# Performance work log

Measured on AMD Instinct MI355X. Metric: run time of the kernel, lower is better.

The kernel has to match this reference:

```python
import jax, jax.numpy as jnp
import numpy as np

HEADS = 8
DIM_HEAD = 64  # note: per-head dim is inner_dim/heads = 512 due to the module's inner_dim = dim_head*dim
SCALE = DIM_HEAD ** (-0.5)
EPS = 1e-5


def layernorm(x, gamma):
    # nn.LayerNorm(dim, elementwise_affine=False) then x * (gamma + 1)
    mu = jnp.mean(x, axis=-1, keepdims=True)
    var = jnp.var(x, axis=-1, keepdims=True)
    xn = (x - mu) * jax.lax.rsqrt(var + EPS)
    return xn * (gamma + 1.0)


def setup_inputs() -> dict:
    key = jax.random.key(0)
    ks = jax.random.split(key, 6)
    b, n, dim = 2, 2048, 256
    inner = DIM_HEAD * dim  # 4096
    x = jax.random.normal(ks[0], (b, n, dim), dtype=jnp.float32)
    gamma = jax.random.normal(ks[1], (dim,), dtype=jnp.float32) * 0.02
    Wq = jax.random.normal(ks[2], (inner, dim), dtype=jnp.float32) * 0.02
    Wk = jax.random.normal(ks[3], (inner, dim), dtype=jnp.float32) * 0.02
    Wv = jax.random.normal(ks[4], (inner, dim), dtype=jnp.float32) * 0.02
    Wo = jax.random.normal(ks[5], (dim, inner), dtype=jnp.float32) * 0.02
    return {"x": x, "gamma": gamma, "Wq": Wq, "Wk": Wk, "Wv": Wv, "Wo": Wo}


def reference(x, gamma, Wq, Wk, Wv, Wo):
    b, n, dim = x.shape
    h = HEADS
    xn = layernorm(x, gamma)  # reuse_attention=True -> norm = LayerNorm(dim)
    # self-attention: context = xn (cross_attend=False, norm_context=Identity)
    q = jnp.einsum('bnd,ed->bne', xn, Wq).reshape(b, n, h, -1).transpose(0, 2, 1, 3)
    k = jnp.einsum('bnd,ed->bne', xn, Wk).reshape(b, n, h, -1).transpose(0, 2, 1, 3)
    v = jnp.einsum('bnd,ed->bne', xn, Wv).reshape(b, n, h, -1).transpose(0, 2, 1, 3)
    qk_sim = jnp.einsum('bhqd,bhkd->bhqk', q * SCALE, k)
    attn = jax.nn.softmax(qk_sim, axis=-1)  # dropout p=0.0 -> identity
    dot = jnp.einsum('bhqk,bhkd->bhqd', attn, v)
    out = dot.transpose(0, 2, 1, 3).reshape(b, n, -1)
    out = jnp.einsum('bne,de->bnd', out, Wo)
    return out
```

## Files before the change

### kernel.cpp

```cpp
#include <hip/hip_runtime.h>


typedef unsigned short u16;
typedef unsigned int u32;
typedef __bf16 bf16x8 __attribute__((ext_vector_type(8)));
typedef float f32x4 __attribute__((ext_vector_type(4)));

__device__ __forceinline__ u16 f2bf(float f) {
    u32 u = __builtin_bit_cast(u32, f);
    u += 0x7fffu + ((u >> 16) & 1u);
    return (u16)(u >> 16);
}

#define GLDS16(G, L)                                                                  \
    __builtin_amdgcn_global_load_lds((const __attribute__((address_space(1))) u32*)(G), \
                                     (__attribute__((address_space(3))) u32*)(L), 16, 0, 0)

template <typename OutT, bool ATOMIC>
__global__ void __launch_bounds__(256, 4) gemm_bt(
    const u16* __restrict__ A, const u16* __restrict__ B, OutT* __restrict__ C,
    int K, int lda, int ldb, int ldc,
    long sAh, long sAb, long sBh, long sBb, long sCh, long sCb,
    int H, int NB, long ksA, long ksB)
{
    __shared__ u16 ldsA[128 * 32];
    __shared__ u16 ldsB[128 * 32];

    const int z = blockIdx.z;
    const int zh = z % H;
    const int zq = z / H;
    const int zb = zq % NB;
    const int kc = zq / NB;
    A += (size_t)zh * sAh + (size_t)zb * sAb + (size_t)kc * ksA;
    B += (size_t)zh * sBh + (size_t)zb * sBb + (size_t)kc * ksB;
    C += (size_t)zh * sCh + (size_t)zb * sCb;

    const int bm = blockIdx.y * 128;
    const int bn = blockIdx.x * 128;
    const int t = threadIdx.x;
    const int w = t >> 6, l = t & 63;
    const int wm = w >> 1, wn = w & 1;
    const int lr = l & 15, lk = l >> 4;
    const int sw = lk ^ ((lr >> 1) & 3);

    const int m0 = t >> 2, s0 = t & 3;
    const int c0 = s0 ^ ((m0 >> 1) & 3);
    const int m1 = 64 + m0;
    const int c1 = s0 ^ ((m1 >> 1) & 3);

    const u16* gA0 = A + (size_t)(bm + m0) * lda + c0 * 8;
    const u16* gA1 = A + (size_t)(bm + m1) * lda + c1 * 8;
    const u16* gB0 = B + (size_t)(bn + m0) * ldb + c0 * 8;
    const u16* gB1 = B + (size_t)(bn + m1) * ldb + c1 * 8;
    u16* lA0 = &ldsA[(t & ~63) * 8];
    u16* lA1 = &ldsA[(256 + (t & ~63)) * 8];
    u16* lB0 = &ldsB[(t & ~63) * 8];
    u16* lB1 = &ldsB[(256 + (t & ~63)) * 8];

    f32x4 acc[4][4];
#pragma unroll
    for (int i = 0; i < 4; ++i)
#pragma unroll
        for (int j = 0; j < 4; ++j)
            acc[i][j] = f32x4{0.f, 0.f, 0.f, 0.f};

    const int nk = K >> 5;
    for (int kt = 0; kt < nk; ++kt) {
        __syncthreads();
        GLDS16(gA0, lA0); GLDS16(gA1, lA1);
        GLDS16(gB0, lB0); GLDS16(gB1, lB1);
        gA0 += 32; gA1 += 32; gB0 += 32; gB1 += 32;
        __syncthreads();

        bf16x8 av[4], bv[4];
#pragma unroll
        for (int i = 0; i < 4; ++i) {
            av[i] = *(const bf16x8*)&ldsA[(wm * 64 + i * 16 + lr) * 32 + sw * 8];
            bv[i] = *(const bf16x8*)&ldsB[(wn * 64 + i * 16 + lr) * 32 + sw * 8];
        }
#pragma unroll
        for (int i = 0; i < 4; ++i)
#pragma unroll
            for (int j = 0; j < 4; ++j)
                acc[i][j] = __builtin_amdgcn_mfma_f32_16x16x32_bf16(av[i], bv[j], acc[i][j], 0, 0, 0);
    }

#pragma unroll
    for (int i = 0; i < 4; ++i) {
        const int row0 = bm + wm * 64 + i * 16 + lk * 4;
#pragma unroll
        for (int j = 0; j < 4; ++j) {
            const int col = bn + wn * 64 + j * 16 + lr;
#pragma unroll
            for (int r = 0; r < 4; ++r) {
                const size_t idx = (size_t)(row0 + r) * ldc + col;
                const float v = acc[i][j][r];
                if constexpr (ATOMIC) {
                    atomicAdd(&C[idx], v);
                } else if constexpr (sizeof(OutT) == 2) {
                    C[idx] = (OutT)f2bf(v);
                } else {
                    C[idx] = (OutT)v;
                }
            }
        }
    }
}

__global__ void __launch_bounds__(256, 2) attn_fused(
    const u16* __restrict__ Y, const u16* __restrict__ xn,
    const u16* __restrict__ Zt, float* __restrict__ out)
{
    __shared__ u16 ldsY[8 * 64 * 32];
    __shared__ u16 ldsB[128 * 32];
    __shared__ u16 ldsZ[256 * 32];
    __shared__ u16 Pl[64 * 136];
    __shared__ float l_lds[64];

    const int i0 = blockIdx.x * 64;
    const int hb = blockIdx.y;
    const int h = hb >> 1, b = hb & 1;

    const int t = threadIdx.x;
    const int w = t >> 6, l = t & 63;
    const int wm = w >> 1, wn = w & 1;
    const int lr = l & 15, lk = l >> 4;
    const int sw = lk ^ ((lr >> 1) & 3);

    if (t < 64) l_lds[t] = 0.f;

    const u16* Yb = Y + (size_t)(b * 2048 + i0) * 2048 + h * 256;
    const u16* xb = xn + (size_t)b * 2048 * 256;
    const u16* Zb = Zt + (size_t)b * 4194304 + (size_t)h * 524288;

#pragma unroll
    for (int p = 0; p < 8; ++p) {
        const int q = p * 256 + t;
        const int kt = q >> 8, qq = q & 255;
        const int m = qq >> 2, s = qq & 3;
        const int c = s ^ ((m >> 1) & 3);
        GLDS16(Yb + (size_t)m * 2048 + kt * 32 + c * 8,
               &ldsY[(p * 256 + (t & ~63)) * 8]);
    }

    const int m0 = t >> 2, s0 = t & 3;
    const int c0 = s0 ^ ((m0 >> 1) & 3);
    const int m1 = 64 + m0;
    const int c1 = s0 ^ ((m1 >> 1) & 3);
    u16* lB0 = &ldsB[(t & ~63) * 8];
    u16* lB1 = &ldsB[(256 + (t & ~63)) * 8];

    const u16 *gZ0, *gZ1, *gZ2, *gZ3;
    u16 *lZ0, *lZ1, *lZ2, *lZ3;
    {
        const int q0 = t, q1 = 256 + t, q2 = 512 + t, q3 = 768 + t;
        const int mz0 = q0 >> 2, mz1 = q1 >> 2, mz2 = q2 >> 2, mz3 = q3 >> 2;
        const int cz0 = (q0 & 3) ^ ((mz0 >> 1) & 3);
        const int cz1 = (q1 & 3) ^ ((mz1 >> 1) & 3);
        const int cz2 = (q2 & 3) ^ ((mz2 >> 1) & 3);
        const int cz3 = (q3 & 3) ^ ((mz3 >> 1) & 3);
        gZ0 = Zb + (size_t)mz0 * 2048 + cz0 * 8;
        gZ1 = Zb + (size_t)mz1 * 2048 + cz1 * 8;
        gZ2 = Zb + (size_t)mz2 * 2048 + cz2 * 8;
        gZ3 = Zb + (size_t)mz3 * 2048 + cz3 * 8;
        lZ0 = &ldsZ[(t & ~63) * 8];
        lZ1 = &ldsZ[(256 + (t & ~63)) * 8];
        lZ2 = &ldsZ[(512 + (t & ~63)) * 8];
        lZ3 = &ldsZ[(768 + (t & ~63)) * 8];
    }

    f32x4 acc_o[2][8];
#pragma unroll
    for (int i = 0; i < 2; ++i)
#pragma unroll
        for (int j = 0; j < 8; ++j)
            acc_o[i][j] = f32x4{0.f, 0.f, 0.f, 0.f};
    float lsum[8];
#pragma unroll
    for (int i = 0; i < 8; ++i) lsum[i] = 0.f;

    __syncthreads();

    for (int jt = 0; jt < 16; ++jt) {
        const int j0 = jt * 128;

        f32x4 acc_s[2][4];
#pragma unroll
        for (int i = 0; i < 2; ++i)
#pragma unroll
            for (int j = 0; j < 4; ++j)
                acc_s[i][j] = f32x4{0.f, 0.f, 0.f, 0.f};

#pragma unroll
        for (int kt = 0; kt < 8; ++kt) {
            __syncthreads();
            GLDS16(xb + (size_t)(j0 + m0) * 256 + kt * 32 + c0 * 8, lB0);
            GLDS16(xb + (size_t)(j0 + m1) * 256 + kt * 32 + c1 * 8, lB1);
            __syncthreads();
            bf16x8 av[2], bv[4];
#pragma unroll
            for (int i = 0; i < 2; ++i)
                av[i] = *(const bf16x8*)&ldsY[kt * 2048 + (wm * 32 + i * 16 + lr) * 32 + sw * 8];
#pragma unroll
            for (int j = 0; j < 4; ++j)
                bv[j] = *(const bf16x8*)&ldsB[(wn * 64 + j * 16 + lr) * 32 + sw * 8];
#pragma unroll
            for (int i = 0; i < 2; ++i)
#pragma unroll
                for (int j = 0; j < 4; ++j)
                    acc_s[i][j] = __builtin_amdgcn_mfma_f32_16x16x32_bf16(av[i], bv[j], acc_s[i][j], 0, 0, 0);
        }

#pragma unroll
        for (int i = 0; i < 2; ++i)
#pragma unroll
            for (int j = 0; j < 4; ++j)
#pragma unroll
                for (int r = 0; r < 4; ++r) {
                    const float e = __expf(acc_s[i][j][r]);
                    lsum[i * 4 + r] += e;
                    Pl[(wm * 32 + i * 16 + lk * 4 + r) * 136 + wn * 64 + j * 16 + lr] = f2bf(e);
                }
        __syncthreads();

#pragma unroll
        for (int kt = 0; kt < 4; ++kt) {
            GLDS16(gZ0 + j0 + kt * 32, lZ0);
            GLDS16(gZ1 + j0 + kt * 32, lZ1);
            GLDS16(gZ2 + j0 + kt * 32, lZ2);
            GLDS16(gZ3 + j0 + kt * 32, lZ3);
            __syncthreads();
            bf16x8 av[2];
#pragma unroll
            for (int i = 0; i < 2; ++i)
                av[i] = *(const bf16x8*)&Pl[(wm * 32 + i * 16 + lr) * 136 + kt * 32 + lk * 8];
#pragma unroll
            for (int jf = 0; jf < 8; ++jf) {
                const bf16x8 bz = *(const bf16x8*)&ldsZ[(wn * 128 + jf * 16 + lr) * 32 + sw * 8];
#pragma unroll
                for (int i = 0; i < 2; ++i)
                    acc_o[i][jf] = __builtin_amdgcn_mfma_f32_16x16x32_bf16(av[i], bz, acc_o[i][jf], 0, 0, 0);
            }
            __syncthreads();
        }
    }

#pragma unroll
    for (int i = 0; i < 2; ++i)
#pragma unroll
        for (int r = 0; r < 4; ++r) {
            float s = lsum[i * 4 + r];
            s += __shfl_xor(s, 1, 64);
            s += __shfl_xor(s, 2, 64);
            s += __shfl_xor(s, 4, 64);
            s += __shfl_xor(s, 8, 64);
            if (lr == 0) atomicAdd(&l_lds[wm * 32 + i * 16 + lk * 4 + r], s);
        }
    __syncthreads();

#pragma unroll
    for (int i = 0; i < 2; ++i)
#pragma unroll
        for (int r = 0; r < 4; ++r) {
            const int row = wm * 32 + i * 16 + lk * 4 + r;
            const float rl = 1.0f / l_lds[row];
            float* orow = out + (size_t)(b * 2048 + i0 + row) * 256 + wn * 128;
#pragma unroll
            for (int jf = 0; jf < 8; ++jf)
                atomicAdd(&orow[jf * 16 + lr], acc_o[i][jf][r] * rl);
        }
}

__global__ void __launch_bounds__(256) tcast3_kernel(const float* __restrict__ Wq,
                                                     const float* __restrict__ Wk,
                                                     const float* __restrict__ Wv,
                                                     u16* __restrict__ dst)
{
    __shared__ u16 tile[64][66];
    const int z = blockIdx.z;
    const int wsel = z >> 3, h = z & 7;
    const float* src = (wsel == 0) ? Wq : (wsel == 1) ? Wk : Wv;
    const float scale = (wsel == 0) ? 0.125f : 1.0f;
    u16* d = dst + (size_t)wsel * 4194304;
    const int d0 = blockIdx.x * 64;
    const int a0 = blockIdx.y * 64;
    const int t = threadIdx.x;
    const int c = t & 63, r0 = t >> 6;
#pragma unroll
    for (int rr = 0; rr < 16; ++rr) {
        const int r = r0 + rr * 4;
        tile[r][c] = f2bf(src[((size_t)h * 2048 + d0 + r) * 256 + a0 + c] * scale);
    }
    __syncthreads();
#pragma unroll
    for (int rr = 0; rr < 16; ++rr) {
        const int r = r0 + rr * 4;
        d[((size_t)h * 256 + a0 + r) * 2048 + d0 + c] = tile[c][r];
    }
}

__global__ void __launch_bounds__(64) ln_kernel(const float* __restrict__ x,
                                                const float* __restrict__ g,
                                                u16* __restrict__ xn)
{
    const size_t row = blockIdx.x;
    const int l = threadIdx.x;
    const float4 v = ((const float4*)(x + row * 256))[l];
    float s = v.x + v.y + v.z + v.w;
    float q = v.x * v.x + v.y * v.y + v.z * v.z + v.w * v.w;
#pragma unroll
    for (int o = 32; o > 0; o >>= 1) {
        s += __shfl_xor(s, o, 64);
        q += __shfl_xor(q, o, 64);
    }
    const float mu = s * (1.0f / 256.0f);
    const float var = q * (1.0f / 256.0f) - mu * mu;
    const float rs = rsqrtf(var + 1e-5f);
    const float4 gg = ((const float4*)g)[l];
    ushort4 o4;
    o4.x = f2bf((v.x - mu) * rs * (gg.x + 1.0f));
    o4.y = f2bf((v.y - mu) * rs * (gg.y + 1.0f));
    o4.z = f2bf((v.z - mu) * rs * (gg.z + 1.0f));
    o4.w = f2bf((v.w - mu) * rs * (gg.w + 1.0f));
    ((ushort4*)(xn + row * 256))[l] = o4;
}

__global__ void __launch_bounds__(256) cast_bf16_kernel(const float* __restrict__ src,
                                                        u16* __restrict__ dst, float scale)
{
    const size_t i = (size_t)blockIdx.x * 256 + threadIdx.x;
    const float4 v = ((const float4*)src)[i];
    ushort4 o4;
    o4.x = f2bf(v.x * scale);
    o4.y = f2bf(v.y * scale);
    o4.z = f2bf(v.z * scale);
    o4.w = f2bf(v.w * scale);
    ((ushort4*)dst)[i] = o4;
}

extern "C" void kernel_launch(void* const* d_in, const int* in_sizes, int n_in,
                              void* d_out, int out_size, void* d_ws, size_t ws_size,
                              hipStream_t stream)
{
    (void)in_sizes; (void)n_in; (void)ws_size;
    const float* x     = (const float*)d_in[0];
    const float* gamma = (const float*)d_in[1];
    const float* Wq    = (const float*)d_in[2];
    const float* Wk    = (const float*)d_in[3];
    const float* Wv    = (const float*)d_in[4];
    const float* Wo    = (const float*)d_in[5];
    float* out = (float*)d_out;

    char* ws = (char*)d_ws;
    const size_t MB = 1048576;
    u16* wqt   = (u16*)(ws);
    u16* wkt   = (u16*)(ws + 8 * MB);
    u16* wvt   = (u16*)(ws + 16 * MB);
    u16* wo    = (u16*)(ws + 24 * MB);
    u16* xn    = (u16*)(ws + 32 * MB);
    u16* Mt    = (u16*)(ws + 34 * MB);
    u16* Nb    = (u16*)(ws + 35 * MB);
    float* MtF = (float*)(ws + 36 * MB);
    float* NbF = (float*)(ws + 38 * MB);
    u16* Y     = (u16*)(ws + 44 * MB);
    u16* Zt    = (u16*)(ws + 60 * MB);

    hipMemsetAsync(d_out, 0, (size_t)out_size * sizeof(float), stream);
    hipMemsetAsync(MtF, 0, 4 * MB, stream);

    tcast3_kernel<<<dim3(32, 4, 24), 256, 0, stream>>>(Wq, Wk, Wv, wqt);
    cast_bf16_kernel<<<4096, 256, 0, stream>>>(Wo, wo, 1.0f);
    ln_kernel<<<4096, 64, 0, stream>>>(x, gamma, xn);

    gemm_bt<float, true><<<dim3(2, 2, 32), 256, 0, stream>>>(
        wkt, wqt, MtF, 512, 2048, 2048, 256,
        524288L, 0, 524288L, 0, 65536L, 0, 8, 1, 512L, 512L);

    gemm_bt<float, true><<<dim3(2, 2, 32), 256, 0, stream>>>(
        wo, wvt, NbF, 512, 16384, 2048, 256,
        2048L, 0, 524288L, 0, 65536L, 0, 8, 1, 512L, 512L);

    cast_bf16_kernel<<<1024, 256, 0, stream>>>(MtF, Mt, 1.0f);

    gemm_bt<u16, false><<<dim3(16, 32, 1), 256, 0, stream>>>(
        xn, Mt, Y, 256, 256, 256, 2048,
        0, 0, 0, 0, 0, 0, 1, 1, 0, 0);

    gemm_bt<u16, false><<<dim3(16, 16, 2), 256, 0, stream>>>(
        Nb, xn, Zt, 256, 256, 256, 2048,
        0, 0, 0, 524288L, 0, 4194304L, 1, 2, 0, 0);

    attn_fused<<<dim3(32, 16), 256, 0, stream>>>(Y, xn, Zt, out);
}
```

Measured before the change: 299.4 us.

## Double-buffer LDS tiles in GEMM and attention kernels, keep Y fragments in registers

```diff
diff --git a/kernel.cpp b/kernel.cpp
--- a/kernel.cpp
+++ b/kernel.cpp
@@ -23,8 +23,8 @@
     long sAh, long sAb, long sBh, long sBb, long sCh, long sCb,
     int H, int NB, long ksA, long ksB)
 {
-    __shared__ u16 ldsA[128 * 32];
-    __shared__ u16 ldsB[128 * 32];
+    __shared__ u16 ldsA[2][128 * 32];
+    __shared__ u16 ldsB[2][128 * 32];
 
     const int z = blockIdx.z;
     const int zh = z % H;
@@ -47,15 +47,13 @@
     const int c0 = s0 ^ ((m0 >> 1) & 3);
     const int m1 = 64 + m0;
     const int c1 = s0 ^ ((m1 >> 1) & 3);
+    const int o0 = (t & ~63) * 8;
+    const int o1 = (256 + (t & ~63)) * 8;
 
     const u16* gA0 = A + (size_t)(bm + m0) * lda + c0 * 8;
     const u16* gA1 = A + (size_t)(bm + m1) * lda + c1 * 8;
     const u16* gB0 = B + (size_t)(bn + m0) * ldb + c0 * 8;
     const u16* gB1 = B + (size_t)(bn + m1) * ldb + c1 * 8;
-    u16* lA0 = &ldsA[(t & ~63) * 8];
-    u16* lA1 = &ldsA[(256 + (t & ~63)) * 8];
-    u16* lB0 = &ldsB[(t & ~63) * 8];
-    u16* lB1 = &ldsB[(256 + (t & ~63)) * 8];
 
     f32x4 acc[4][4];
 #pragma unroll
@@ -65,24 +63,31 @@
             acc[i][j] = f32x4{0.f, 0.f, 0.f, 0.f};
 
     const int nk = K >> 5;
+
+    GLDS16(gA0, &ldsA[0][o0]); GLDS16(gA1, &ldsA[0][o1]);
+    GLDS16(gB0, &ldsB[0][o0]); GLDS16(gB1, &ldsB[0][o1]);
+    gA0 += 32; gA1 += 32; gB0 += 32; gB1 += 32;
+    __syncthreads();
+
     for (int kt = 0; kt < nk; ++kt) {
-        __syncthreads();
-        GLDS16(gA0, lA0); GLDS16(gA1, lA1);
-        GLDS16(gB0, lB0); GLDS16(gB1, lB1);
-        gA0 += 32; gA1 += 32; gB0 += 32; gB1 += 32;
-        __syncthreads();
-
+        const int cb = kt & 1;
+        if (kt + 1 < nk) {
+            GLDS16(gA0, &ldsA[cb ^ 1][o0]); GLDS16(gA1, &ldsA[cb ^ 1][o1]);
+            GLDS16(gB0, &ldsB[cb ^ 1][o0]); GLDS16(gB1, &ldsB[cb ^ 1][o1]);
+            gA0 += 32; gA1 += 32; gB0 += 32; gB1 += 32;
+        }
         bf16x8 av[4], bv[4];
 #pragma unroll
         for (int i = 0; i < 4; ++i) {
-            av[i] = *(const bf16x8*)&ldsA[(wm * 64 + i * 16 + lr) * 32 + sw * 8];
-            bv[i] = *(const bf16x8*)&ldsB[(wn * 64 + i * 16 + lr) * 32 + sw * 8];
+            av[i] = *(const bf16x8*)&ldsA[cb][(wm * 64 + i * 16 + lr) * 32 + sw * 8];
+            bv[i] = *(const bf16x8*)&ldsB[cb][(wn * 64 + i * 16 + lr) * 32 + sw * 8];
         }
 #pragma unroll
         for (int i = 0; i < 4; ++i)
 #pragma unroll
             for (int j = 0; j < 4; ++j)
                 acc[i][j] = __builtin_amdgcn_mfma_f32_16x16x32_bf16(av[i], bv[j], acc[i][j], 0, 0, 0);
+        if (kt + 1 < nk) __syncthreads();
     }
 
 #pragma unroll
@@ -111,9 +116,8 @@
     const u16* __restrict__ Y, const u16* __restrict__ xn,
     const u16* __restrict__ Zt, float* __restrict__ out)
 {
-    __shared__ u16 ldsY[8 * 64 * 32];
-    __shared__ u16 ldsB[128 * 32];
-    __shared__ u16 ldsZ[256 * 32];
+    __shared__ u16 ldsB[2][128 * 32];
+    __shared__ u16 ldsZ[2][256 * 32];
     __shared__ u16 Pl[64 * 136];
     __shared__ float l_lds[64];
 
@@ -133,25 +137,18 @@
     const u16* xb = xn + (size_t)b * 2048 * 256;
     const u16* Zb = Zt + (size_t)b * 4194304 + (size_t)h * 524288;
 
-#pragma unroll
-    for (int p = 0; p < 8; ++p) {
-        const int q = p * 256 + t;
-        const int kt = q >> 8, qq = q & 255;
-        const int m = qq >> 2, s = qq & 3;
-        const int c = s ^ ((m >> 1) & 3);
-        GLDS16(Yb + (size_t)m * 2048 + kt * 32 + c * 8,
-               &ldsY[(p * 256 + (t & ~63)) * 8]);
-    }
-
     const int m0 = t >> 2, s0 = t & 3;
     const int c0 = s0 ^ ((m0 >> 1) & 3);
     const int m1 = 64 + m0;
     const int c1 = s0 ^ ((m1 >> 1) & 3);
-    u16* lB0 = &ldsB[(t & ~63) * 8];
-    u16* lB1 = &ldsB[(256 + (t & ~63)) * 8];
+    const int oB0 = (t & ~63) * 8;
+    const int oB1 = (256 + (t & ~63)) * 8;
 
     const u16 *gZ0, *gZ1, *gZ2, *gZ3;
-    u16 *lZ0, *lZ1, *lZ2, *lZ3;
+    const int oZ0 = (t & ~63) * 8;
+    const int oZ1 = (256 + (t & ~63)) * 8;
+    const int oZ2 = (512 + (t & ~63)) * 8;
+    const int oZ3 = (768 + (t & ~63)) * 8;
     {
         const int q0 = t, q1 = 256 + t, q2 = 512 + t, q3 = 768 + t;
         const int mz0 = q0 >> 2, mz1 = q1 >> 2, mz2 = q2 >> 2, mz3 = q3 >> 2;
@@ -163,11 +160,28 @@
         gZ1 = Zb + (size_t)mz1 * 2048 + cz1 * 8;
         gZ2 = Zb + (size_t)mz2 * 2048 + cz2 * 8;
         gZ3 = Zb + (size_t)mz3 * 2048 + cz3 * 8;
-        lZ0 = &ldsZ[(t & ~63) * 8];
-        lZ1 = &ldsZ[(256 + (t & ~63)) * 8];
-        lZ2 = &ldsZ[(512 + (t & ~63)) * 8];
-        lZ3 = &ldsZ[(768 + (t & ~63)) * 8];
-    }
+    }
+
+    u16* ldsY = &ldsZ[0][0];
+#pragma unroll
+    for (int p = 0; p < 8; ++p) {
+        const int q = p * 256 + t;
+        const int kt = q >> 8, qq = q & 255;
+        const int m = qq >> 2, s = qq & 3;
+        const int c = s ^ ((m >> 1) & 3);
+        GLDS16(Yb + (size_t)m * 2048 + kt * 32 + c * 8,
+               &ldsY[(p * 256 + (t & ~63)) * 8]);
+    }
+    GLDS16(xb + (size_t)m0 * 256 + c0 * 8, &ldsB[0][oB0]);
+    GLDS16(xb + (size_t)m1 * 256 + c1 * 8, &ldsB[0][oB1]);
+    __syncthreads();
+
+    bf16x8 yr[8][2];
+#pragma unroll
+    for (int kt = 0; kt < 8; ++kt)
+#pragma unroll
+        for (int i = 0; i < 2; ++i)
+            yr[kt][i] = *(const bf16x8*)&ldsY[kt * 2048 + (wm * 32 + i * 16 + lr) * 32 + sw * 8];
 
     f32x4 acc_o[2][8];
 #pragma unroll
@@ -179,8 +193,6 @@
 #pragma unroll
     for (int i = 0; i < 8; ++i) lsum[i] = 0.f;
 
-    __syncthreads();
-
     for (int jt = 0; jt < 16; ++jt) {
         const int j0 = jt * 128;
 
@@ -193,22 +205,26 @@
 
 #pragma unroll
         for (int kt = 0; kt < 8; ++kt) {
-            __syncthreads();
-            GLDS16(xb + (size_t)(j0 + m0) * 256 + kt * 32 + c0 * 8, lB0);
-            GLDS16(xb + (size_t)(j0 + m1) * 256 + kt * 32 + c1 * 8, lB1);
-            __syncthreads();
-            bf16x8 av[2], bv[4];
+            const int cb = kt & 1;
+            if (kt < 7) {
+                GLDS16(xb + (size_t)(j0 + m0) * 256 + (kt + 1) * 32 + c0 * 8, &ldsB[cb ^ 1][oB0]);
+                GLDS16(xb + (size_t)(j0 + m1) * 256 + (kt + 1) * 32 + c1 * 8, &ldsB[cb ^ 1][oB1]);
+            } else {
+                GLDS16(gZ0 + j0, &ldsZ[0][oZ0]);
+                GLDS16(gZ1 + j0, &ldsZ[0][oZ1]);
+                GLDS16(gZ2 + j0, &ldsZ[0][oZ2]);
+                GLDS16(gZ3 + j0, &ldsZ[0][oZ3]);
+            }
+            bf16x8 bv[4];
+#pragma unroll
+            for (int j = 0; j < 4; ++j)
+                bv[j] = *(const bf16x8*)&ldsB[cb][(wn * 64 + j * 16 + lr) * 32 + sw * 8];
 #pragma unroll
             for (int i = 0; i < 2; ++i)
-                av[i] = *(const bf16x8*)&ldsY[kt * 2048 + (wm * 32 + i * 16 + lr) * 32 + sw * 8];
-#pragma unroll
-            for (int j = 0; j < 4; ++j)
-                bv[j] = *(const bf16x8*)&ldsB[(wn * 64 + j * 16 + lr) * 32 + sw * 8];
-#pragma unroll
-            for (int i = 0; i < 2; ++i)
 #pragma unroll
                 for (int j = 0; j < 4; ++j)
-                    acc_s[i][j] = __builtin_amdgcn_mfma_f32_16x16x32_bf16(av[i], bv[j], acc_s[i][j], 0, 0, 0);
+                    acc_s[i][j] = __builtin_amdgcn_mfma_f32_16x16x32_bf16(yr[kt][i], bv[j], acc_s[i][j], 0, 0, 0);
+            if (kt < 7) __syncthreads();
         }
 
 #pragma unroll
@@ -225,18 +241,23 @@
 
 #pragma unroll
         for (int kt = 0; kt < 4; ++kt) {
-            GLDS16(gZ0 + j0 + kt * 32, lZ0);
-            GLDS16(gZ1 + j0 + kt * 32, lZ1);
-            GLDS16(gZ2 + j0 + kt * 32, lZ2);
-            GLDS16(gZ3 + j0 + kt * 32, lZ3);
-            __syncthreads();
+            const int cz = kt & 1;
+            if (kt < 3) {
+                GLDS16(gZ0 + j0 + (kt + 1) * 32, &ldsZ[cz ^ 1][oZ0]);
+                GLDS16(gZ1 + j0 + (kt + 1) * 32, &ldsZ[cz ^ 1][oZ1]);
+                GLDS16(gZ2 + j0 + (kt + 1) * 32, &ldsZ[cz ^ 1][oZ2]);
+                GLDS16(gZ3 + j0 + (kt + 1) * 32, &ldsZ[cz ^ 1][oZ3]);
+            } else if (jt < 15) {
+                GLDS16(xb + (size_t)(j0 + 128 + m0) * 256 + c0 * 8, &ldsB[0][oB0]);
+                GLDS16(xb + (size_t)(j0 + 128 + m1) * 256 + c1 * 8, &ldsB[0][oB1]);
+            }
             bf16x8 av[2];
 #pragma unroll
             for (int i = 0; i < 2; ++i)
                 av[i] = *(const bf16x8*)&Pl[(wm * 32 + i * 16 + lr) * 136 + kt * 32 + lk * 8];
 #pragma unroll
             for (int jf = 0; jf < 8; ++jf) {
-                const bf16x8 bz = *(const bf16x8*)&ldsZ[(wn * 128 + jf * 16 + lr) * 32 + sw * 8];
+                const bf16x8 bz = *(const bf16x8*)&ldsZ[cz][(wn * 128 + jf * 16 + lr) * 32 + sw * 8];
 #pragma unroll
                 for (int i = 0; i < 2; ++i)
                     acc_o[i][jf] = __builtin_amdgcn_mfma_f32_16x16x32_bf16(av[i], bz, acc_o[i][jf], 0, 0, 0);
```

Result: faster. 283.2 us (-5.4%).
